# Kernel tuning notes

Hardware: AMD Instinct MI355X
Metric: run time of the kernel (lower is better)

The kernel has to match this reference:

```python
import jax, jax.numpy as jnp
import numpy as np

QLEN, BSZ, HID, NH, HD = 512, 8, 1024, 16, 64
PLEN = 2 * QLEN
SCALE = 1.0 / (HD ** 0.5)
BIG_NUM = 1e30
EPS = 1e-5


def _rel_shift(x, klen):
    # x: [b, n, i, j] -> shifted [b, n, i, klen], same raw-reshape trick as torch.
    b, n, i, j = x.shape
    x = x.reshape(b, n, j, i)[:, :, 1:, :]
    x = x.reshape(b, n, i, j - 1)
    return x[:, :, :, :klen]


def setup_inputs() -> dict:
    key = jax.random.key(0)
    ks = jax.random.split(key, 12)
    s = jnp.float32(0.02)
    return {
        "hidden_states": jax.random.normal(ks[0], (QLEN, BSZ, HID), jnp.float32),
        "position_embed": jax.random.normal(ks[1], (PLEN, BSZ, HID), jnp.float32),
        "segment_embed": jax.random.uniform(ks[2], (QLEN, QLEN, BSZ, 2), jnp.float32),
        "attn_mask": jnp.zeros((QLEN, QLEN, BSZ, 1), jnp.float32),
        "q": jax.random.normal(ks[3], (HID, NH, HD), jnp.float32) * s,
        "k": jax.random.normal(ks[4], (HID, NH, HD), jnp.float32) * s,
        "v": jax.random.normal(ks[5], (HID, NH, HD), jnp.float32) * s,
        "r": jax.random.normal(ks[6], (HID, NH, HD), jnp.float32) * s,
        "o": jax.random.normal(ks[7], (HID, NH, HD), jnp.float32) * s,
        "r_w_bias": jax.random.normal(ks[8], (NH, HD), jnp.float32) * s,
        "r_r_bias": jax.random.normal(ks[9], (NH, HD), jnp.float32) * s,
        "r_s_bias": jax.random.normal(ks[10], (NH, HD), jnp.float32) * s,
        "seg_mat": jax.random.normal(ks[11], (2, NH, HD), jnp.float32) * s,
        "ln_gamma": jnp.ones((HID,), jnp.float32),
        "ln_beta": jnp.zeros((HID,), jnp.float32),
    }


def reference(hidden_states, position_embed, segment_embed, attn_mask,
              q, k, v, r, o, r_w_bias, r_r_bias, r_s_bias, seg_mat,
              ln_gamma, ln_beta):
    query = jnp.einsum('ibh,hnd->ibnd', hidden_states, q)
    key_ = jnp.einsum('ibh,hnd->ibnd', hidden_states, k)
    value = jnp.einsum('ibh,hnd->ibnd', hidden_states, v)
    key_r = jnp.einsum('ibh,hnd->ibnd', position_embed, r)

    # content score
    ac = jnp.einsum('ibnd,jbnd->bnij', query + r_w_bias, key_)
    # relative position score with rel_shift
    bd = jnp.einsum('ibnd,jbnd->bnij', query + r_r_bias, key_r)
    bd = _rel_shift(bd, ac.shape[3])
    # segment score
    ef = jnp.einsum('ibnd,snd->ibns', query + r_s_bias, seg_mat)
    ef = jnp.einsum('ijbs,ibns->bnij', segment_embed, ef)

    attn_score = (ac + bd + ef) * SCALE
    attn_score = attn_score - BIG_NUM * jnp.transpose(attn_mask, (2, 3, 0, 1))
    attn_prob = jax.nn.softmax(attn_score, axis=-1)  # dropout is identity in eval

    attn_out = jnp.einsum('bnij,jbnd->ibnd', attn_prob, value)
    attn_out = jnp.einsum('ibnd,hnd->ibh', attn_out, o)

    x = attn_out + hidden_states
    mu = jnp.mean(x, axis=-1, keepdims=True)
    var = jnp.mean((x - mu) ** 2, axis=-1, keepdims=True)
    return (x - mu) * jax.lax.rsqrt(var + EPS) * ln_gamma + ln_beta
```

## Files before the change

kernel.cpp:

```cpp
#include <hip/hip_runtime.h>
#include <hip/hip_bf16.h>

#define I_LEN 512
#define BSZ   8
#define HIDN  1024
#define NHEAD 16
#define HDIM  64
#define PLEN_ 1024
#define SCALE_F 0.125f
#define BIGNUM 1e30f
#define LN_EPS 1e-5f

typedef unsigned int   u32;
typedef unsigned short u16;
typedef __attribute__((ext_vector_type(8))) short bf16x8;
typedef __attribute__((ext_vector_type(4))) float f32x4;

__device__ __forceinline__ float bflo(u32 w) { return __uint_as_float(w << 16); }
__device__ __forceinline__ float bfhi(u32 w) { return __uint_as_float(w & 0xffff0000u); }
__device__ __forceinline__ u16 f2bf(float x) {
  u32 u = __float_as_uint(x);
  return (u16)((u + 0x7fffu + ((u >> 16) & 1u)) >> 16);
}
__device__ __forceinline__ void bf8_to_f(const uint4 v, float* f) {
  f[0] = bflo(v.x); f[1] = bfhi(v.x);
  f[2] = bflo(v.y); f[3] = bfhi(v.y);
  f[4] = bflo(v.z); f[5] = bfhi(v.z);
  f[6] = bflo(v.w); f[7] = bfhi(v.w);
}

#define GLOAD_LDS16(gp, lp) __builtin_amdgcn_global_load_lds( \
    (const __attribute__((address_space(1))) void*)(gp),      \
    (__attribute__((address_space(3))) void*)(lp), 16, 0, 0)

__global__ __launch_bounds__(256)
void proj_gemm(const u16* __restrict__ Hb, const float* __restrict__ pos,
               const u16* __restrict__ Wqt, const u16* __restrict__ Wkt,
               const u16* __restrict__ Wvt, const u16* __restrict__ Wrt,
               u16* __restrict__ Qh, u16* __restrict__ Kf,
               u16* __restrict__ Vh, u16* __restrict__ Krf) {
  constexpr int K = 1024;
  __shared__ union {
    struct { u16 As[128 * 64]; u16 Bs[128 * 64]; } st;
    u16 epi[4][64 * 68];
    u16 epiK[128 * 137];
  } sm;
  u16* As = sm.st.As;
  u16* Bs = sm.st.Bs;
  const int id = blockIdx.x;
  const int low = id & 7;
  const int rest = id >> 3;
  const int bx = rest & 7;
  const int grp = low + 8 * (rest >> 3);
  const int by = grp & 31;
  const int z = grp >> 5;
  const u16* Bt; u16* C;
  if (z == 0)      { Bt = Wqt; C = Qh;  }
  else if (z == 1) { Bt = Wkt; C = Kf;  }
  else if (z == 2) { Bt = Wvt; C = Vh;  }
  else if (z == 3) { Bt = Wrt; C = Krf; }
  else             { Bt = Wrt; C = Krf; }
  const float* Apos = pos + (size_t)((z == 4) ? 4096 : 0) * 1024;
  const int bm = by * 128, bn = bx * 128;
  const int tid = threadIdx.x, wv = tid >> 6, lane = tid & 63;
  const int l15 = lane & 15, g = lane >> 4;
  const int wr = wv >> 1, wc = wv & 1;

  f32x4 acc[4][4];
#pragma unroll
  for (int m = 0; m < 4; ++m)
#pragma unroll
    for (int n = 0; n < 4; ++n) acc[m][n] = (f32x4){0.f, 0.f, 0.f, 0.f};

  for (int k0 = 0; k0 < K; k0 += 64) {
#pragma unroll
    for (int p = 0; p < 4; ++p) {
      const int unit = (wv * 4 + p) * 64 + lane;
      const int row = unit >> 3, up = unit & 7, c = up ^ (row & 7);
      GLOAD_LDS16(&Bt[(size_t)(bn + row) * K + k0 + c * 8], &Bs[unit * 8]);
    }
    if (z < 3) {
#pragma unroll
      for (int p = 0; p < 4; ++p) {
        const int unit = (wv * 4 + p) * 64 + lane;
        const int row = unit >> 3, up = unit & 7, c = up ^ (row & 7);
        GLOAD_LDS16(&Hb[(size_t)(bm + row) * K + k0 + c * 8], &As[unit * 8]);
      }
    } else {
#pragma unroll
      for (int p = 0; p < 4; ++p) {
        const int unit = p * 256 + tid;
        const int row = unit >> 3, up = unit & 7, c = up ^ (row & 7);
        const float* src = &Apos[(size_t)(bm + row) * K + k0 + c * 8];
        const float4 f0 = *(const float4*)src;
        const float4 f1 = *(const float4*)(src + 4);
        ushort4 h0, h1;
        h0.x = f2bf(f0.x); h0.y = f2bf(f0.y); h0.z = f2bf(f0.z); h0.w = f2bf(f0.w);
        h1.x = f2bf(f1.x); h1.y = f2bf(f1.y); h1.z = f2bf(f1.z); h1.w = f2bf(f1.w);
        *(ushort4*)&As[unit * 8] = h0;
        *(ushort4*)&As[unit * 8 + 4] = h1;
      }
    }
    __syncthreads();
#pragma unroll
    for (int h = 0; h < 2; ++h) {
      bf16x8 af[4], bfv[4];
#pragma unroll
      for (int m = 0; m < 4; ++m) {
        const int row = wr * 64 + m * 16 + l15;
        af[m] = *(const bf16x8*)&As[row * 64 + ((h * 4 + g) ^ (row & 7)) * 8];
      }
#pragma unroll
      for (int n = 0; n < 4; ++n) {
        const int col = wc * 64 + n * 16 + l15;
        bfv[n] = *(const bf16x8*)&Bs[col * 64 + ((h * 4 + g) ^ (col & 7)) * 8];
      }
#pragma unroll
      for (int m = 0; m < 4; ++m)
#pragma unroll
        for (int n = 0; n < 4; ++n)
          acc[m][n] = __builtin_amdgcn_mfma_f32_16x16x32_bf16(af[m], bfv[n], acc[m][n], 0, 0, 0);
    }
    __syncthreads();
  }
  if (z == 1 || z >= 3) {
    u16* E128 = sm.epiK;
#pragma unroll
    for (int m = 0; m < 4; ++m)
#pragma unroll
      for (int nf = 0; nf < 4; ++nf)
#pragma unroll
        for (int r = 0; r < 4; ++r)
          E128[(wr * 64 + m * 16 + g * 4 + r) * 137 + wc * 64 + nf * 16 + l15] =
              f2bf(acc[m][nf][r]);
    __syncthreads();
    const int tK = (z == 1) ? by : (by + ((z == 4) ? 32 : 0));
    const int TS = (z == 1) ? 32 : 64;
#pragma unroll
    for (int q = 0; q < 8; ++q) {
      const int rid = wv * 8 + q;
      const int n_loc = rid >> 4, b_ = (rid >> 1) & 7, h = rid & 1;
      union { u16 us[8]; uint4 qv; } o;
#pragma unroll
      for (int e = 0; e < 8; ++e)
        o.us[e] = E128[(l15 * 8 + b_) * 137 + n_loc * 64 + h * 32 + g * 8 + e];
      const int head = bx * 2 + n_loc;
      const size_t base = (((size_t)(b_ * 16 + head) * TS + tK) * 2 + h) * 512 + lane * 8;
      *(uint4*)&C[base] = o.qv;
    }
  } else {
    u16* slice = sm.epi[wv];
    __syncthreads();
#pragma unroll
    for (int m = 0; m < 4; ++m)
#pragma unroll
      for (int nf = 0; nf < 4; ++nf)
#pragma unroll
        for (int r = 0; r < 4; ++r)
          slice[(m * 16 + g * 4 + r) * 68 + nf * 16 + l15] = f2bf(acc[m][nf][r]);
#pragma unroll
    for (int it = 0; it < 8; ++it) {
      const int rl = it * 8 + (lane >> 3);
      const int cl = (lane & 7) * 8;
      const ushort4 a = *(const ushort4*)&slice[rl * 68 + cl];
      const ushort4 b2 = *(const ushort4*)&slice[rl * 68 + cl + 4];
      const int row = bm + wr * 64 + rl;
      const int col = bn + wc * 64 + cl;
      const size_t idx = ((size_t)((row & 7) * 16 + (col >> 6)) * 512 + (row >> 3)) * 64 + (col & 63);
      *(ushort4*)&C[idx] = a;
      *(ushort4*)&C[idx + 4] = b2;
    }
  }
}

__global__ __launch_bounds__(256)
void vrepack_kernel(u16* __restrict__ V) {
  __shared__ u16 tile[64][72];
  const int bn = blockIdx.x, slab = blockIdx.y;
  const int t = threadIdx.x;
  const size_t base = ((size_t)bn * 8 + slab) * 4096;
  {
    const int jl = t >> 2, c0 = (t & 3) * 16;
    const uint4 v0 = *(const uint4*)&V[base + jl * 64 + c0];
    const uint4 v1 = *(const uint4*)&V[base + jl * 64 + c0 + 8];
    *(uint4*)&tile[jl][c0] = v0;
    *(uint4*)&tile[jl][c0 + 8] = v1;
  }
  __syncthreads();
  const int lane = t & 63, g = lane >> 4, l15 = lane & 15;
#pragma unroll
  for (int w = 0; w < 2; ++w) {
    const int run = w * 4 + (t >> 6);
    const int c = run >> 1, h = run & 1;
    union { u16 us[8]; uint4 qv; } o;
#pragma unroll
    for (int e = 0; e < 8; ++e) o.us[e] = tile[h * 32 + g * 8 + e][16 * c + l15];
    *(uint4*)&V[base + run * 512 + lane * 8] = o.qv;
  }
}

__global__ __launch_bounds__(256)
void hcvt_kernel(const float* __restrict__ hidden, const float* __restrict__ ow,
                 u16* __restrict__ Hb, u16* __restrict__ Wob) {
  const size_t i = (size_t)blockIdx.x * 256 + threadIdx.x;
  const float* src; u16* dst; size_t off;
  if (i < 524288) { src = hidden; dst = Hb; off = i * 8; }
  else            { src = ow;     dst = Wob; off = (i - 524288) * 8; }
  const float4 a = *(const float4*)&src[off];
  const float4 b = *(const float4*)&src[off + 4];
  ushort4 o0, o1;
  o0.x = f2bf(a.x); o0.y = f2bf(a.y); o0.z = f2bf(a.z); o0.w = f2bf(a.w);
  o1.x = f2bf(b.x); o1.y = f2bf(b.y); o1.z = f2bf(b.z); o1.w = f2bf(b.w);
  *(ushort4*)&dst[off] = o0;
  *(ushort4*)&dst[off + 4] = o1;
}

__global__ __launch_bounds__(256)
void wtrans_kernel(const float* __restrict__ W0, const float* __restrict__ W1,
                   const float* __restrict__ W2, const float* __restrict__ W3,
                   u16* __restrict__ T0, u16* __restrict__ T1,
                   u16* __restrict__ T2, u16* __restrict__ T3) {
  __shared__ u16 tile[64][72];
  const int z = blockIdx.z;
  const float* W = (z == 0) ? W0 : ((z == 1) ? W1 : ((z == 2) ? W2 : W3));
  u16* T = (z == 0) ? T0 : ((z == 1) ? T1 : ((z == 2) ? T2 : T3));
  const int h0 = blockIdx.y * 64, nd0 = blockIdx.x * 64;
  const int t = threadIdx.x;
  {
    const int hr = t >> 2, c0 = (t & 3) * 16;
#pragma unroll
    for (int q = 0; q < 4; ++q) {
      const float4 f = *(const float4*)&W[(size_t)(h0 + hr) * 1024 + nd0 + c0 + q * 4];
      tile[hr][c0 + q * 4 + 0] = f2bf(f.x);
      tile[hr][c0 + q * 4 + 1] = f2bf(f.y);
      tile[hr][c0 + q * 4 + 2] = f2bf(f.z);
      tile[hr][c0 + q * 4 + 3] = f2bf(f.w);
    }
  }
  __syncthreads();
  const int ndr = t >> 2, hc0 = (t & 3) * 16;
  union { u16 us[16]; uint4 qv[2]; } o;
#pragma unroll
  for (int e = 0; e < 16; ++e) o.us[e] = tile[hc0 + e][ndr];
  uint4* dst = (uint4*)&T[(size_t)(nd0 + ndr) * 1024 + h0 + hc0];
  dst[0] = o.qv[0]; dst[1] = o.qv[1];
}

__global__ __launch_bounds__(256)
void setrans_kernel(const float* __restrict__ sege, const float* __restrict__ amask,
                    u16* __restrict__ SE4, u16* __restrict__ MK) {
  const int i = blockIdx.x;
  const int j = blockIdx.y * 256 + threadIdx.x;
  const float* sp = &sege[((size_t)i * 512 + j) * 16];
  const float* mp = &amask[((size_t)i * 512 + j) * 8];
  float se[16], mk[8];
#pragma unroll
  for (int q = 0; q < 4; ++q) {
    const float4 f = *(const float4*)(sp + q * 4);
    se[q * 4 + 0] = f.x; se[q * 4 + 1] = f.y; se[q * 4 + 2] = f.z; se[q * 4 + 3] = f.w;
  }
#pragma unroll
  for (int q = 0; q < 2; ++q) {
    const float4 f = *(const float4*)(mp + q * 4);
    mk[q * 4 + 0] = f.x; mk[q * 4 + 1] = f.y; mk[q * 4 + 2] = f.z; mk[q * 4 + 3] = f.w;
  }
#pragma unroll
  for (int b = 0; b < 8; ++b) {
    const u32 pk = (u32)f2bf(se[b * 2]) | ((u32)f2bf(se[b * 2 + 1]) << 16);
    const size_t plane = ((size_t)b * 512 + i) * 512 + j;
    *(u32*)&SE4[plane * 2] = pk;
    MK[plane] = f2bf(BIGNUM * mk[b]);
  }
}

__global__ __launch_bounds__(256)
void seg_e_kernel(const u16* __restrict__ Qh, const float* __restrict__ rsb,
                  const float* __restrict__ segm, float* __restrict__ E) {
  const int gt = blockIdx.x * 256 + threadIdx.x;
  const int i = gt >> 7, bb = (gt >> 4) & 7, n = gt & 15;
  const size_t base = (((size_t)bb * 16 + n) * 512 + i) * 64;
  float e0 = 0.f, e1 = 0.f;
#pragma unroll
  for (int u8 = 0; u8 < 8; ++u8) {
    const uint4 qv = *(const uint4*)&Qh[base + u8 * 8];
    float qf[8];
    bf8_to_f(qv, qf);
#pragma unroll
    for (int w = 0; w < 8; ++w) {
      const int d = u8 * 8 + w;
      const float q = qf[w] + rsb[n * HDIM + d];
      e0 += q * segm[n * HDIM + d];
      e1 += q * segm[HIDN + n * HDIM + d];
    }
  }
  E[(size_t)gt * 2 + 0] = e0;
  E[(size_t)gt * 2 + 1] = e1;
}

__global__ __launch_bounds__(256)
void attn_mfma(const u16* __restrict__ Qh, const u16* __restrict__ Kf,
               const u16* __restrict__ Vf, const u16* __restrict__ Krf,
               const float* __restrict__ E, const u16* __restrict__ SE4,
               const u16* __restrict__ MK, const float* __restrict__ rwb,
               const float* __restrict__ rrb, u16* __restrict__ AOb) {
  __shared__ u16 Pl[4][16 * 64];
  const int id = blockIdx.x;
  const int b = id & 7, n = (id >> 3) & 15;
  const int i0 = (id >> 7) * 64;
  const int bn = b * 16 + n;
  const int t = threadIdx.x, wv = t >> 6, lane = t & 63;
  const int l15 = lane & 15, g = lane >> 4;
  const int irow0 = i0 + wv * 16;
  u16* Pw = Pl[wv];
  const int bn64 = bn * 64;

  bf16x8 qcf[2], qrf[2];
#pragma unroll
  for (int h = 0; h < 2; ++h) {
    const int d0 = 32 * h + g * 8;
    const uint4 qv = *(const uint4*)&Qh[((size_t)bn * 512 + irow0 + l15) * 64 + d0];
    float qf[8]; bf8_to_f(qv, qf);
    union { u16 us[8]; bf16x8 v; } ua, ub;
#pragma unroll
    for (int w = 0; w < 8; ++w) {
      ua.us[w] = f2bf((qf[w] + rwb[n * HDIM + d0 + w]) * SCALE_F);
      ub.us[w] = f2bf((qf[w] + rrb[n * HDIM + d0 + w]) * SCALE_F);
    }
    qcf[h] = ua.v; qrf[h] = ub.v;
  }

  float e0v[4], e1v[4], lrun[4];
  f32x4 accO[4];
#pragma unroll
  for (int r = 0; r < 4; ++r) {
    const int i = irow0 + 4 * g + r;
    const float2 ee = *(const float2*)&E[((size_t)(i * BSZ + b) * NHEAD + n) * 2];
    e0v[r] = ee.x * SCALE_F; e1v[r] = ee.y * SCALE_F;
    lrun[r] = 0.f;
  }
#pragma unroll
  for (int c = 0; c < 4; ++c) accO[c] = (f32x4){0.f, 0.f, 0.f, 0.f};

  for (int jb = 0; jb < I_LEN; jb += 64) {
    u32 sev[4][4]; u16 mkv[4][4];
#pragma unroll
    for (int c = 0; c < 4; ++c)
#pragma unroll
      for (int r = 0; r < 4; ++r) {
        const size_t plane = ((size_t)b * 512 + (irow0 + 4 * g + r)) * 512 + jb + 16 * c + l15;
        sev[c][r] = *(const u32*)&SE4[plane * 2];
        mkv[c][r] = MK[plane];
      }
    bf16x8 vf[4][2];
#pragma unroll
    for (int c = 0; c < 4; ++c) {
      const u16* vp = &Vf[((((size_t)bn * 8 + (jb >> 6)) * 4 + c) * 2) * 512 + lane * 8];
      vf[c][0] = *(const bf16x8*)vp;
      vf[c][1] = *(const bf16x8*)(vp + 512);
    }
    f32x4 S[4];
#pragma unroll
    for (int c = 0; c < 4; ++c) S[c] = (f32x4){0.f, 0.f, 0.f, 0.f};
#pragma unroll
    for (int c = 0; c < 4; ++c) {
      const u16* kp = &Kf[(((size_t)bn * 32 + (jb >> 4) + c) * 2) * 512 + lane * 8];
      S[c] = __builtin_amdgcn_mfma_f32_16x16x32_bf16(qcf[0], *(const bf16x8*)kp, S[c], 0, 0, 0);
      S[c] = __builtin_amdgcn_mfma_f32_16x16x32_bf16(qcf[1], *(const bf16x8*)(kp + 512), S[c], 0, 0, 0);
    }
    const int tb = (jb + 496 - irow0) >> 4;
    f32x4 T[5];
#pragma unroll
    for (int c = 0; c < 5; ++c) T[c] = (f32x4){0.f, 0.f, 0.f, 0.f};
#pragma unroll
    for (int c = 0; c < 5; ++c) {
      const u16* kp = &Krf[(((size_t)bn * 64 + tb + c) * 2) * 512 + lane * 8];
      T[c] = __builtin_amdgcn_mfma_f32_16x16x32_bf16(qrf[0], *(const bf16x8*)kp, T[c], 0, 0, 0);
      T[c] = __builtin_amdgcn_mfma_f32_16x16x32_bf16(qrf[1], *(const bf16x8*)(kp + 512), T[c], 0, 0, 0);
    }
    float bd[4][4];
#pragma unroll
    for (int r = 0; r < 4; ++r) {
      const int ii = 4 * g + r;
      const int pos = (lane & 48) | ((l15 - ii) & 15);
      float bp[5];
#pragma unroll
      for (int c = 0; c < 5; ++c) bp[c] = __shfl(T[c][r], pos, 64);
      const bool sel = l15 >= ii;
#pragma unroll
      for (int c = 0; c < 4; ++c) bd[c][r] = sel ? bp[c + 1] : bp[c];
    }
#pragma unroll
    for (int c = 0; c < 4; ++c)
#pragma unroll
      for (int r = 0; r < 4; ++r) {
        const u32 sev_ = sev[c][r];
        const float s = S[c][r] + bd[c][r] + bflo(sev_) * e0v[r] + bfhi(sev_) * e1v[r]
                        - bflo((u32)mkv[c][r]);
        const float p = __expf(s);
        S[c][r] = p;
        lrun[r] += p;
      }
#pragma unroll
    for (int c = 0; c < 4; ++c)
#pragma unroll
      for (int r = 0; r < 4; ++r) {
        const int ii = 4 * g + r;
        Pw[ii * 64 + ((16 * c + l15) ^ ((ii & 7) << 3))] = f2bf(S[c][r]);
      }
    const bf16x8 pa0 = *(const bf16x8*)&Pw[l15 * 64 + ((g * 8) ^ ((l15 & 7) << 3))];
    const bf16x8 pa1 = *(const bf16x8*)&Pw[l15 * 64 + ((32 + g * 8) ^ ((l15 & 7) << 3))];
#pragma unroll
    for (int c = 0; c < 4; ++c) {
      accO[c] = __builtin_amdgcn_mfma_f32_16x16x32_bf16(pa0, vf[c][0], accO[c], 0, 0, 0);
      accO[c] = __builtin_amdgcn_mfma_f32_16x16x32_bf16(pa1, vf[c][1], accO[c], 0, 0, 0);
    }
  }
#pragma unroll
  for (int r = 0; r < 4; ++r) {
#pragma unroll
    for (int o = 1; o < 16; o <<= 1) lrun[r] += __shfl_xor(lrun[r], o);
  }
#pragma unroll
  for (int c = 0; c < 4; ++c)
#pragma unroll
    for (int r = 0; r < 4; ++r) {
      const int ii = 4 * g + r;
      AOb[(size_t)(irow0 + ii) * 8192 + bn64 + 16 * c + l15] = f2bf(accO[c][r] / lrun[r]);
    }
}

__global__ __launch_bounds__(256)
void oproj_gemm(const u16* __restrict__ A, const u16* __restrict__ Wob,
                const float* __restrict__ Res, float* __restrict__ C) {
  constexpr int K = 1024;
  __shared__ u16 As[64 * 64];
  __shared__ u16 Bs[128 * 64];
  const int id = blockIdx.x;
  const int low = id & 7;
  const int rest = id >> 3;
  const int bx = rest & 7;
  const int by = low + 8 * (rest >> 3);
  const int bm = by * 64, bn = bx * 128;
  const int tid = threadIdx.x, wv = tid >> 6, lane = tid & 63;
  const int l15 = lane & 15, g = lane >> 4;
  const int wr = wv >> 1, wc = wv & 1;

  f32x4 acc[2][4];
#pragma unroll
  for (int m = 0; m < 2; ++m)
#pragma unroll
    for (int n = 0; n < 4; ++n) acc[m][n] = (f32x4){0.f, 0.f, 0.f, 0.f};

  for (int k0 = 0; k0 < K; k0 += 64) {
#pragma unroll
    for (int p = 0; p < 2; ++p) {
      const int unit = (wv * 2 + p) * 64 + lane;
      const int row = unit >> 3, up = unit & 7, c = up ^ (row & 7);
      GLOAD_LDS16(&A[(size_t)(bm + row) * K + k0 + c * 8], &As[unit * 8]);
    }
#pragma unroll
    for (int p = 0; p < 4; ++p) {
      const int unit = (wv * 4 + p) * 64 + lane;
      const int row = unit >> 3, up = unit & 7, c = up ^ (row & 7);
      GLOAD_LDS16(&Wob[(size_t)(bn + row) * K + k0 + c * 8], &Bs[unit * 8]);
    }
    __syncthreads();
#pragma unroll
    for (int h = 0; h < 2; ++h) {
      bf16x8 af[2], bfv[4];
#pragma unroll
      for (int m = 0; m < 2; ++m) {
        const int row = wr * 32 + m * 16 + l15;
        af[m] = *(const bf16x8*)&As[row * 64 + ((h * 4 + g) ^ (row & 7)) * 8];
      }
#pragma unroll
      for (int n = 0; n < 4; ++n) {
        const int col = wc * 64 + n * 16 + l15;
        bfv[n] = *(const bf16x8*)&Bs[col * 64 + ((h * 4 + g) ^ (col & 7)) * 8];
      }
#pragma unroll
      for (int m = 0; m < 2; ++m)
#pragma unroll
        for (int n = 0; n < 4; ++n)
          acc[m][n] = __builtin_amdgcn_mfma_f32_16x16x32_bf16(af[m], bfv[n], acc[m][n], 0, 0, 0);
    }
    __syncthreads();
  }
#pragma unroll
  for (int m = 0; m < 2; ++m) {
    const int row0 = bm + wr * 32 + m * 16 + g * 4;
#pragma unroll
    for (int nf = 0; nf < 4; ++nf) {
      const int col = bn + wc * 64 + nf * 16 + l15;
#pragma unroll
      for (int r = 0; r < 4; ++r) {
        const int row = row0 + r;
        C[(size_t)row * 1024 + col] = acc[m][nf][r] + Res[(size_t)row * 1024 + col];
      }
    }
  }
}

__global__ __launch_bounds__(256)
void ln_kernel(const float* __restrict__ X, const float* __restrict__ gam,
               const float* __restrict__ bet, float* __restrict__ out) {
  const int row = blockIdx.x, t = threadIdx.x;
  const float4 x4 = *(const float4*)&X[(size_t)row * HIDN + t * 4];
  float s  = x4.x + x4.y + x4.z + x4.w;
  float sq = x4.x * x4.x + x4.y * x4.y + x4.z * x4.z + x4.w * x4.w;
#pragma unroll
  for (int o = 32; o >= 1; o >>= 1) { s += __shfl_xor(s, o); sq += __shfl_xor(sq, o); }
  __shared__ float red[8];
  const int wv = t >> 6;
  if ((t & 63) == 0) { red[wv * 2] = s; red[wv * 2 + 1] = sq; }
  __syncthreads();
  s  = red[0] + red[2] + red[4] + red[6];
  sq = red[1] + red[3] + red[5] + red[7];
  const float mu  = s * (1.f / HIDN);
  const float var = sq * (1.f / HIDN) - mu * mu;
  const float rs  = rsqrtf(var + LN_EPS);
  const float4 g4 = *(const float4*)&gam[t * 4];
  const float4 b4 = *(const float4*)&bet[t * 4];
  float4 o4;
  o4.x = (x4.x - mu) * rs * g4.x + b4.x;
  o4.y = (x4.y - mu) * rs * g4.y + b4.y;
  o4.z = (x4.z - mu) * rs * g4.z + b4.z;
  o4.w = (x4.w - mu) * rs * g4.w + b4.w;
  *(float4*)&out[(size_t)row * HIDN + t * 4] = o4;
}

extern "C" void kernel_launch(void* const* d_in, const int* in_sizes, int n_in,
                              void* d_out, int out_size, void* d_ws, size_t ws_size,
                              hipStream_t stream) {
  (void)in_sizes; (void)n_in; (void)out_size; (void)ws_size;
  const float* hidden = (const float*)d_in[0];
  const float* pos    = (const float*)d_in[1];
  const float* sege   = (const float*)d_in[2];
  const float* amask  = (const float*)d_in[3];
  const float* qw     = (const float*)d_in[4];
  const float* kw     = (const float*)d_in[5];
  const float* vw     = (const float*)d_in[6];
  const float* rw     = (const float*)d_in[7];
  const float* ow     = (const float*)d_in[8];
  const float* rwb    = (const float*)d_in[9];
  const float* rrb    = (const float*)d_in[10];
  const float* rsb    = (const float*)d_in[11];
  const float* segm   = (const float*)d_in[12];
  const float* gam    = (const float*)d_in[13];
  const float* bet    = (const float*)d_in[14];
  float* out = (float*)d_out;
  char* ws = (char*)d_ws;

  const size_t MiB = 1ull << 20;
  u16*   Wqt = (u16*)(ws);
  u16*   Wkt = (u16*)(ws + 2 * MiB);
  u16*   Wvt = (u16*)(ws + 4 * MiB);
  u16*   Wrt = (u16*)(ws + 6 * MiB);
  u16*   AOb = (u16*)(ws);
  u16*   Qh  = (u16*)(ws + 8 * MiB);
  u16*   Kf  = (u16*)(ws + 16 * MiB);
  u16*   Vf  = (u16*)(ws + 24 * MiB);
  u16*   Krf = (u16*)(ws + 32 * MiB);
  float* X   = (float*)(ws + 32 * MiB);
  u16*   Hb  = (u16*)(ws + 48 * MiB);
  u16*   SE4 = (u16*)(ws + 48 * MiB);
  u16*   MK  = (u16*)(ws + 56 * MiB);
  float* E   = (float*)(ws + 60 * MiB);
  u16*   Wob = (u16*)(ws + 60 * MiB + 512 * 1024);

  wtrans_kernel<<<dim3(16, 16, 4), 256, 0, stream>>>(qw, kw, vw, rw, Wqt, Wkt, Wvt, Wrt);
  hcvt_kernel<<<2560, 256, 0, stream>>>(hidden, ow, Hb, Wob);
  proj_gemm<<<1280, 256, 0, stream>>>(Hb, pos, Wqt, Wkt, Wvt, Wrt, Qh, Kf, Vf, Krf);
  vrepack_kernel<<<dim3(128, 8), 256, 0, stream>>>(Vf);
  setrans_kernel<<<dim3(512, 2), 256, 0, stream>>>(sege, amask, SE4, MK);
  seg_e_kernel<<<256, 256, 0, stream>>>(Qh, rsb, segm, E);
  attn_mfma<<<1024, 256, 0, stream>>>(Qh, Kf, Vf, Krf, E, SE4, MK, rwb, rrb, AOb);
  oproj_gemm<<<512, 256, 0, stream>>>(AOb, Wob, hidden, X);
  ln_kernel<<<4096, 256, 0, stream>>>(X, gam, bet, out);
}
```

Measured before the change: 168.7 us.

## Double-buffer LDS tiles in projection and output GEMMs

The projection and output-projection GEMMs now use two LDS buffers. Each iteration issues global-to-LDS loads for the next k-tile before running MFMAs on the current one, which removes one barrier per iteration and overlaps memory latency with compute. This doubles LDS usage per block, which may lower occupancy. For the fp32 position path the loads go through registers, so some of that overlap depends on the compiler's scheduling.

```diff
diff --git a/kernel.cpp b/kernel.cpp
--- a/kernel.cpp
+++ b/kernel.cpp
@@ -41,7 +41,7 @@
                u16* __restrict__ Vh, u16* __restrict__ Krf) {
   constexpr int K = 1024;
   __shared__ union {
-    struct { u16 As[128 * 64]; u16 Bs[128 * 64]; } st;
+    struct { u16 As[2 * 8192]; u16 Bs[2 * 8192]; } st;
     u16 epi[4][64 * 68];
     u16 epiK[128 * 137];
   } sm;
@@ -66,54 +66,68 @@
   const int l15 = lane & 15, g = lane >> 4;
   const int wr = wv >> 1, wc = wv & 1;
 
+#define STAGE_B_P(BUF, K0)                                                    \
+  _Pragma("unroll")                                                           \
+  for (int p = 0; p < 4; ++p) {                                               \
+    const int unit = (wv * 4 + p) * 64 + lane;                                \
+    const int row = unit >> 3, up = unit & 7, cc = up ^ (row & 7);            \
+    GLOAD_LDS16(&Bt[(size_t)(bn + row) * K + (K0) + cc * 8],                  \
+                &Bs[(BUF) * 8192 + unit * 8]);                                \
+  }
+#define STAGE_A16_P(BUF, K0)                                                  \
+  _Pragma("unroll")                                                           \
+  for (int p = 0; p < 4; ++p) {                                               \
+    const int unit = (wv * 4 + p) * 64 + lane;                                \
+    const int row = unit >> 3, up = unit & 7, cc = up ^ (row & 7);            \
+    GLOAD_LDS16(&Hb[(size_t)(bm + row) * K + (K0) + cc * 8],                  \
+                &As[(BUF) * 8192 + unit * 8]);                                \
+  }
+#define STAGE_A32_P(BUF, K0)                                                  \
+  _Pragma("unroll")                                                           \
+  for (int p = 0; p < 4; ++p) {                                               \
+    const int unit = p * 256 + tid;                                           \
+    const int row = unit >> 3, up = unit & 7, cc = up ^ (row & 7);            \
+    const float* src = &Apos[(size_t)(bm + row) * K + (K0) + cc * 8];         \
+    const float4 f0 = *(const float4*)src;                                    \
+    const float4 f1 = *(const float4*)(src + 4);                              \
+    ushort4 h0, h1;                                                           \
+    h0.x = f2bf(f0.x); h0.y = f2bf(f0.y); h0.z = f2bf(f0.z); h0.w = f2bf(f0.w); \
+    h1.x = f2bf(f1.x); h1.y = f2bf(f1.y); h1.z = f2bf(f1.z); h1.w = f2bf(f1.w); \
+    *(ushort4*)&As[(BUF) * 8192 + unit * 8] = h0;                             \
+    *(ushort4*)&As[(BUF) * 8192 + unit * 8 + 4] = h1;                         \
+  }
+
   f32x4 acc[4][4];
 #pragma unroll
   for (int m = 0; m < 4; ++m)
 #pragma unroll
     for (int n = 0; n < 4; ++n) acc[m][n] = (f32x4){0.f, 0.f, 0.f, 0.f};
 
-  for (int k0 = 0; k0 < K; k0 += 64) {
-#pragma unroll
-    for (int p = 0; p < 4; ++p) {
-      const int unit = (wv * 4 + p) * 64 + lane;
-      const int row = unit >> 3, up = unit & 7, c = up ^ (row & 7);
-      GLOAD_LDS16(&Bt[(size_t)(bn + row) * K + k0 + c * 8], &Bs[unit * 8]);
-    }
-    if (z < 3) {
-#pragma unroll
-      for (int p = 0; p < 4; ++p) {
-        const int unit = (wv * 4 + p) * 64 + lane;
-        const int row = unit >> 3, up = unit & 7, c = up ^ (row & 7);
-        GLOAD_LDS16(&Hb[(size_t)(bm + row) * K + k0 + c * 8], &As[unit * 8]);
-      }
-    } else {
-#pragma unroll
-      for (int p = 0; p < 4; ++p) {
-        const int unit = p * 256 + tid;
-        const int row = unit >> 3, up = unit & 7, c = up ^ (row & 7);
-        const float* src = &Apos[(size_t)(bm + row) * K + k0 + c * 8];
-        const float4 f0 = *(const float4*)src;
-        const float4 f1 = *(const float4*)(src + 4);
-        ushort4 h0, h1;
-        h0.x = f2bf(f0.x); h0.y = f2bf(f0.y); h0.z = f2bf(f0.z); h0.w = f2bf(f0.w);
-        h1.x = f2bf(f1.x); h1.y = f2bf(f1.y); h1.z = f2bf(f1.z); h1.w = f2bf(f1.w);
-        *(ushort4*)&As[unit * 8] = h0;
-        *(ushort4*)&As[unit * 8 + 4] = h1;
-      }
-    }
-    __syncthreads();
+  STAGE_B_P(0, 0);
+  if (z < 3) { STAGE_A16_P(0, 0); } else { STAGE_A32_P(0, 0); }
+  __syncthreads();
+
+  int cur = 0;
+  for (int t = 0; t < 16; ++t) {
+    if (t + 1 < 16) {
+      const int k1 = (t + 1) * 64;
+      STAGE_B_P(cur ^ 1, k1);
+      if (z < 3) { STAGE_A16_P(cur ^ 1, k1); } else { STAGE_A32_P(cur ^ 1, k1); }
+    }
+    const u16* Ac = &As[cur * 8192];
+    const u16* Bc = &Bs[cur * 8192];
 #pragma unroll
     for (int h = 0; h < 2; ++h) {
       bf16x8 af[4], bfv[4];
 #pragma unroll
       for (int m = 0; m < 4; ++m) {
         const int row = wr * 64 + m * 16 + l15;
-        af[m] = *(const bf16x8*)&As[row * 64 + ((h * 4 + g) ^ (row & 7)) * 8];
+        af[m] = *(const bf16x8*)&Ac[row * 64 + ((h * 4 + g) ^ (row & 7)) * 8];
       }
 #pragma unroll
       for (int n = 0; n < 4; ++n) {
         const int col = wc * 64 + n * 16 + l15;
-        bfv[n] = *(const bf16x8*)&Bs[col * 64 + ((h * 4 + g) ^ (col & 7)) * 8];
+        bfv[n] = *(const bf16x8*)&Bc[col * 64 + ((h * 4 + g) ^ (col & 7)) * 8];
       }
 #pragma unroll
       for (int m = 0; m < 4; ++m)
@@ -122,7 +136,9 @@
           acc[m][n] = __builtin_amdgcn_mfma_f32_16x16x32_bf16(af[m], bfv[n], acc[m][n], 0, 0, 0);
     }
     __syncthreads();
-  }
+    cur ^= 1;
+  }
+
   if (z == 1 || z >= 3) {
     u16* E128 = sm.epiK;
 #pragma unroll
@@ -433,8 +449,8 @@
 void oproj_gemm(const u16* __restrict__ A, const u16* __restrict__ Wob,
                 const float* __restrict__ Res, float* __restrict__ C) {
   constexpr int K = 1024;
-  __shared__ u16 As[64 * 64];
-  __shared__ u16 Bs[128 * 64];
+  __shared__ u16 As[2 * 4096];
+  __shared__ u16 Bs[2 * 8192];
   const int id = blockIdx.x;
   const int low = id & 7;
   const int rest = id >> 3;
@@ -445,38 +461,47 @@
   const int l15 = lane & 15, g = lane >> 4;
   const int wr = wv >> 1, wc = wv & 1;
 
+#define STAGE_O(BUF, K0)                                                      \
+  _Pragma("unroll")                                                           \
+  for (int p = 0; p < 2; ++p) {                                               \
+    const int unit = (wv * 2 + p) * 64 + lane;                                \
+    const int row = unit >> 3, up = unit & 7, cc = up ^ (row & 7);            \
+    GLOAD_LDS16(&A[(size_t)(bm + row) * K + (K0) + cc * 8],                   \
+                &As[(BUF) * 4096 + unit * 8]);                                \
+  }                                                                           \
+  _Pragma("unroll")                                                           \
+  for (int p = 0; p < 4; ++p) {                                               \
+    const int unit = (wv * 4 + p) * 64 + lane;                                \
+    const int row = unit >> 3, up = unit & 7, cc = up ^ (row & 7);            \
+    GLOAD_LDS16(&Wob[(size_t)(bn + row) * K + (K0) + cc * 8],                 \
+                &Bs[(BUF) * 8192 + unit * 8]);                                \
+  }
+
   f32x4 acc[2][4];
 #pragma unroll
   for (int m = 0; m < 2; ++m)
 #pragma unroll
     for (int n = 0; n < 4; ++n) acc[m][n] = (f32x4){0.f, 0.f, 0.f, 0.f};
 
-  for (int k0 = 0; k0 < K; k0 += 64) {
-#pragma unroll
-    for (int p = 0; p < 2; ++p) {
-      const int unit = (wv * 2 + p) * 64 + lane;
-      const int row = unit >> 3, up = unit & 7, c = up ^ (row & 7);
-      GLOAD_LDS16(&A[(size_t)(bm + row) * K + k0 + c * 8], &As[unit * 8]);
-    }
-#pragma unroll
-    for (int p = 0; p < 4; ++p) {
-      const int unit = (wv * 4 + p) * 64 + lane;
-      const int row = unit >> 3, up = unit & 7, c = up ^ (row & 7);
-      GLOAD_LDS16(&Wob[(size_t)(bn + row) * K + k0 + c * 8], &Bs[unit * 8]);
-    }
-    __syncthreads();
+  STAGE_O(0, 0);
+  __syncthreads();
+  int cur = 0;
+  for (int t = 0; t < 16; ++t) {
+    if (t + 1 < 16) { STAGE_O(cur ^ 1, (t + 1) * 64); }
+    const u16* Ac = &As[cur * 4096];
+    const u16* Bc = &Bs[cur * 8192];
 #pragma unroll
     for (int h = 0; h < 2; ++h) {
       bf16x8 af[2], bfv[4];
 #pragma unroll
       for (int m = 0; m < 2; ++m) {
         const int row = wr * 32 + m * 16 + l15;
-        af[m] = *(const bf16x8*)&As[row * 64 + ((h * 4 + g) ^ (row & 7)) * 8];
+        af[m] = *(const bf16x8*)&Ac[row * 64 + ((h * 4 + g) ^ (row & 7)) * 8];
       }
 #pragma unroll
       for (int n = 0; n < 4; ++n) {
         const int col = wc * 64 + n * 16 + l15;
-        bfv[n] = *(const bf16x8*)&Bs[col * 64 + ((h * 4 + g) ^ (col & 7)) * 8];
+        bfv[n] = *(const bf16x8*)&Bc[col * 64 + ((h * 4 + g) ^ (col & 7)) * 8];
       }
 #pragma unroll
       for (int m = 0; m < 2; ++m)
@@ -485,6 +510,7 @@
           acc[m][n] = __builtin_amdgcn_mfma_f32_16x16x32_bf16(af[m], bfv[n], acc[m][n], 0, 0, 0);
     }
     __syncthreads();
+    cur ^= 1;
   }
 #pragma unroll
   for (int m = 0; m < 2; ++m) {
```

Result: faster. 165.2 us (-2.1%).
